# Kernel tuning notes

Hardware: AMD Instinct MI355X
Metric: run time of the kernel (lower is better)

## Reference

```python
import jax, jax.numpy as jnp
import numpy as np
from math import sqrt

N = 50000
E = 800000
D_EMB = 512
DK = 64
DV = 64
HEADS = 8


def setup_inputs() -> dict:
    key = jax.random.key(0)
    k1, k2, k3, k4 = jax.random.split(key, 4)
    x = jax.random.normal(k1, (N, D_EMB), dtype=jnp.float32)
    edge_index = jax.random.randint(k2, (2, E), 0, N, dtype=jnp.int64)
    out_qkv = (2 * DK + DV) * HEADS  # 1536
    W_qkv = jax.random.normal(k3, (out_qkv, D_EMB), dtype=jnp.float32) / sqrt(D_EMB)
    b_qkv = jnp.zeros((out_qkv,), dtype=jnp.float32)
    W_ff = jax.random.normal(k4, (D_EMB, DV * HEADS), dtype=jnp.float32) / sqrt(DV * HEADS)
    b_ff = jnp.zeros((D_EMB,), dtype=jnp.float32)
    return {"x": x, "edge_index": edge_index, "W_qkv": W_qkv, "b_qkv": b_qkv,
            "W_ff": W_ff, "b_ff": b_ff}


def _attention_message(Q, K, V, senders, receivers, n_nodes):
    # Q,K: [N, H, dK], V: [N, H, dV]; edge lists: [E]
    scale = 1.0 / sqrt(Q.shape[-1])
    # per-edge scores: [E, H]
    scores = jnp.einsum('ehd,ehd->eh', Q[receivers], K[senders]) * scale
    # segment softmax over incoming edges of each receiver
    smax = jax.ops.segment_max(scores, receivers, num_segments=n_nodes)  # [N, H]
    ex = jnp.exp(scores - smax[receivers])                               # [E, H]
    denom = jax.ops.segment_sum(ex, receivers, num_segments=n_nodes)    # [N, H]
    att = ex / denom[receivers]                                         # [E, H]
    # weighted scatter of V from senders to receivers: [N, H, dV]
    out = jax.ops.segment_sum(att[:, :, None] * V[senders], receivers,
                              num_segments=n_nodes)
    return out, att


def reference(x, edge_index, W_qkv, b_qkv, W_ff, b_ff):
    n_nodes = x.shape[0]
    qkv = x @ W_qkv.T + b_qkv  # [N, (2*dK+dV)*H]
    Q, K, V = jnp.split(qkv, [DK * HEADS, 2 * DK * HEADS], axis=-1)
    Q = Q.reshape(n_nodes, HEADS, DK)
    K = K.reshape(n_nodes, HEADS, DK)
    V = V.reshape(n_nodes, HEADS, DV)
    senders, receivers = edge_index[0], edge_index[1]
    msg, _ = _attention_message(Q, K, V, senders, receivers, n_nodes)
    # aggregate_heads: flatten heads and project to d_Embedding
    out = msg.reshape(n_nodes, HEADS * DV) @ W_ff.T + b_ff
    return out
```

## Files before the change

### kernel.cpp

```cpp
#include <hip/hip_runtime.h>

static constexpr int NN = 50000;
static constexpr int NE = 800000;
static constexpr int DEMB = 512;
static constexpr int QKV_OUT = 1536;

typedef _Float16 half8 __attribute__((ext_vector_type(8)));
typedef float floatx4 __attribute__((ext_vector_type(4)));

#define KQ_SCALE (127.0f / 5.5f)
#define KQ_DEQ   (5.5f / 127.0f)

static constexpr size_t OFF_QH   = 0;
static constexpr size_t OFF_KV8  = 51200000;
static constexpr size_t OFF_MSG  = 102400000;
static constexpr size_t OFF_SRT  = 153600000;
static constexpr size_t OFF_DEG  = 156800000;
static constexpr size_t OFF_OFFA = 157000000;
static constexpr size_t OFF_CUR  = 157200064;
static constexpr size_t OFF_FLAG = 157400064;
static constexpr size_t OFF_WQH  = 157400128;
static constexpr size_t OFF_WFH  = 158972992;

typedef __attribute__((address_space(1))) const void* gas_ptr;
typedef __attribute__((address_space(3))) void* lds_ptr_t;

__device__ __forceinline__ void load_lds16(const void* g, void* l) {
  __builtin_amdgcn_global_load_lds((gas_ptr)g, (lds_ptr_t)l, 16, 0, 0);
}

__global__ __launch_bounds__(256)
void k_cvt(const float* __restrict__ in, _Float16* __restrict__ out, int n8) {
  int i = blockIdx.x * 256 + threadIdx.x;
  if (i < n8) {
    floatx4 a = *(const floatx4*)(in + (size_t)i * 8);
    floatx4 b = *(const floatx4*)(in + (size_t)i * 8 + 4);
    half8 h;
    #pragma unroll
    for (int q = 0; q < 4; ++q) { h[q] = (_Float16)a[q]; h[q + 4] = (_Float16)b[q]; }
    *(half8*)(out + (size_t)i * 8) = h;
  }
}

__global__ __launch_bounds__(64)
void k_detect64(const void* __restrict__ edge, int* __restrict__ flag) {
  if (threadIdx.x == 0) {
    const int* p = (const int*)edge;
    int is64 = 1;
    for (int i = 0; i < 16; ++i) if (p[2 * i + 1] != 0) is64 = 0;
    *flag = is64;
  }
}

__device__ __forceinline__ int edge_at(const void* edge, int row, int e, int is64) {
  if (is64) return (int)((const long long*)edge)[(size_t)row * NE + e];
  return ((const int*)edge)[(size_t)row * NE + e];
}

__global__ __launch_bounds__(1024)
void k_scan(const int* __restrict__ deg, int* __restrict__ off,
            int* __restrict__ cur, int n) {
  __shared__ int sums[1024];
  int tid = threadIdx.x;
  int per = (n + 1023) >> 10;
  int start = tid * per;
  int end = start + per; if (end > n) end = n;
  int s = 0;
  for (int i = start; i < end; ++i) s += deg[i];
  sums[tid] = s;
  __syncthreads();
  for (int d = 1; d < 1024; d <<= 1) {
    int v = (tid >= d) ? sums[tid - d] : 0;
    __syncthreads();
    sums[tid] += v;
    __syncthreads();
  }
  int run = (tid == 0) ? 0 : sums[tid - 1];
  for (int i = start; i < end; ++i) {
    off[i] = run; cur[i] = run; run += deg[i];
  }
  if (tid == 0) off[n] = sums[1023];
}

__global__ __launch_bounds__(256)
void k_scatter(const void* __restrict__ edge, const int* __restrict__ flag,
               int* __restrict__ cur, int* __restrict__ srt) {
  int e = blockIdx.x * 256 + threadIdx.x;
  if (e < NE) {
    int is64 = *flag;
    int r = edge_at(edge, 1, e, is64);
    int s = edge_at(edge, 0, e, is64);
    int pos = atomicAdd(&cur[r], 1);
    srt[pos] = s;
  }
}

template<int MODE>
__global__ __launch_bounds__(512, 2)
void k_gemmB(const _Float16* __restrict__ Ah, const _Float16* __restrict__ Bh,
             const float* __restrict__ bias,
             void* __restrict__ out0, void* __restrict__ out1,
             const void* __restrict__ edge, const int* __restrict__ flag,
             int* __restrict__ deg,
             int M, int N, int K, int nxt, int gemmBlocks) {
  __shared__ _Float16 Bs[128 * 512];
  const int tid = threadIdx.x;

  if (MODE == 0 && blockIdx.x >= gemmBlocks) {
    int e = (blockIdx.x - gemmBlocks) * 512 + tid;
    if (e < NE) {
      int r = edge_at(edge, 1, e, *flag);
      atomicAdd(&deg[r], 1);
    }
    return;
  }

  const int cpx = gemmBlocks >> 3;
  const int w = (blockIdx.x & 7) * cpx + (blockIdx.x >> 3);
  const int m0 = (w / nxt) * 512;
  const int n0 = (w % nxt) * 128;

  const int wid = tid >> 6, lane = tid & 63;
  const int fr = lane & 15;
  const int fs = lane >> 4;

  #pragma unroll
  for (int it = 0; it < 16; ++it) {
    int L = it * 512 + tid;
    int row = L >> 6, sc = L & 63;
    int c = sc ^ (row & 7);
    load_lds16(Bh + (size_t)(n0 + row) * K + c * 8, (char*)Bs + (size_t)L * 16);
  }

  floatx4 acc[4][8];
  #pragma unroll
  for (int m = 0; m < 4; ++m)
    #pragma unroll
    for (int n = 0; n < 8; ++n)
      #pragma unroll
      for (int q = 0; q < 4; ++q) acc[m][n][q] = 0.f;

  int arow[4];
  #pragma unroll
  for (int m = 0; m < 4; ++m) {
    int r = m0 + wid * 64 + m * 16 + fr;
    arow[m] = r < M ? r : M - 1;
  }

  __syncthreads();

  auto LDA = [&](half8* dst, int t) {
    const int k0 = t * 32 + fs * 8;
    #pragma unroll
    for (int m = 0; m < 4; ++m)
      dst[m] = *(const half8*)(Ah + (size_t)arow[m] * K + k0);
  };

  half8 a[4], an[4];
  LDA(a, 0);
  for (int t = 0; t < 16; ++t) {
    if (t + 1 < 16) LDA(an, t + 1);
    half8 b[8];
    #pragma unroll
    for (int n = 0; n < 8; ++n) {
      int R = n * 16 + fr;
      int c = (t * 4 + fs) ^ (R & 7);
      b[n] = *(const half8*)(Bs + R * 512 + c * 8);
    }
    #pragma unroll
    for (int m = 0; m < 4; ++m)
      #pragma unroll
      for (int n = 0; n < 8; ++n)
        acc[m][n] = __builtin_amdgcn_mfma_f32_16x16x32_f16(a[m], b[n], acc[m][n], 0, 0, 0);
    #pragma unroll
    for (int m = 0; m < 4; ++m) a[m] = an[m];
  }

  const int fq = fs << 2;
  #pragma unroll
  for (int m = 0; m < 4; ++m) {
    #pragma unroll
    for (int n = 0; n < 8; ++n) {
      int gn = n0 + n * 16 + fr;
      float bv = bias[gn];
      #pragma unroll
      for (int q = 0; q < 4; ++q) {
        int gm = m0 + wid * 64 + m * 16 + fq + q;
        if (gm < M) {
          float val = acc[m][n][q] + bv;
          if (MODE == 0) {
            int region = gn >> 9;
            int d = gn & 511;
            if (region == 0) {
              ((_Float16*)out0)[(size_t)gm * 512 + d] = (_Float16)val;
            } else {
              float s = fminf(fmaxf(val * KQ_SCALE, -127.f), 127.f);
              signed char c = (signed char)__float2int_rn(s);
              size_t idx = (size_t)gm * 1024 + ((d >> 3) << 4) + (d & 7)
                         + (region == 2 ? 8 : 0);
              ((signed char*)out1)[idx] = c;
            }
          } else {
            ((float*)out0)[(size_t)gm * N + gn] = val;
          }
        }
      }
    }
  }
}

__global__ __launch_bounds__(256)
void k_attn(const _Float16* __restrict__ Qh, const unsigned char* __restrict__ KV8,
            const int* __restrict__ off, const int* __restrict__ srt,
            _Float16* __restrict__ msg) {
  int r = blockIdx.x * 4 + (threadIdx.x >> 6);
  if (r >= NN) return;
  int lane = threadIdx.x & 63;
  int qoff = lane * 8;

  half8 qh = *(const half8*)(Qh + (size_t)r * 512 + qoff);
  float q[8];
  #pragma unroll
  for (int i = 0; i < 8; ++i) q[i] = (float)qh[i] * 0.125f * KQ_DEQ;

  float denom = 0.f;
  float acc[8];
  #pragma unroll
  for (int i = 0; i < 8; ++i) acc[i] = 0.f;

  int e0 = off[r], e1 = off[r + 1];
  if (e1 <= e0) {
    half8 z = {};
    *(half8*)(msg + (size_t)r * 512 + qoff) = z;
    return;
  }

  auto gload = [&](uint4& kv, int s) {
    kv = *(const uint4*)(KV8 + (size_t)s * 1024 + lane * 16);
  };
  auto consume = [&](uint4 kv) {
    int xw = (int)kv.x, yw = (int)kv.y;
    float p = 0.f;
    p += q[0] * (float)((xw << 24) >> 24);
    p += q[1] * (float)((xw << 16) >> 24);
    p += q[2] * (float)((xw << 8) >> 24);
    p += q[3] * (float)(xw >> 24);
    p += q[4] * (float)((yw << 24) >> 24);
    p += q[5] * (float)((yw << 16) >> 24);
    p += q[6] * (float)((yw << 8) >> 24);
    p += q[7] * (float)(yw >> 24);
    p += __shfl_xor(p, 1);
    p += __shfl_xor(p, 2);
    p += __shfl_xor(p, 4);
    float w = __expf(p);
    denom += w;
    int vx = (int)kv.z, vy = (int)kv.w;
    acc[0] += w * (float)((vx << 24) >> 24);
    acc[1] += w * (float)((vx << 16) >> 24);
    acc[2] += w * (float)((vx << 8) >> 24);
    acc[3] += w * (float)(vx >> 24);
    acc[4] += w * (float)((vy << 24) >> 24);
    acc[5] += w * (float)((vy << 16) >> 24);
    acc[6] += w * (float)((vy << 8) >> 24);
    acc[7] += w * (float)(vy >> 24);
  };
  auto sidx = [&](int e) { return srt[e < e1 ? e : e1 - 1]; };

  uint4 b0, b1, b2, b3;
  gload(b0, sidx(e0));
  gload(b1, sidx(e0 + 1));
  gload(b2, sidx(e0 + 2));
  gload(b3, sidx(e0 + 3));
  int sn0 = sidx(e0 + 4), sn1 = sidx(e0 + 5), sn2 = sidx(e0 + 6), sn3 = sidx(e0 + 7);

  int e = e0;
  for (; e + 4 <= e1; e += 4) {
    consume(b0); gload(b0, sn0);
    consume(b1); gload(b1, sn1);
    consume(b2); gload(b2, sn2);
    consume(b3); gload(b3, sn3);
    sn0 = sidx(e + 8); sn1 = sidx(e + 9); sn2 = sidx(e + 10); sn3 = sidx(e + 11);
  }
  int rem = e1 - e;
  if (rem > 0) consume(b0);
  if (rem > 1) consume(b1);
  if (rem > 2) consume(b2);

  float inv = KQ_DEQ / denom;
  half8 oh;
  #pragma unroll
  for (int i = 0; i < 8; ++i) oh[i] = (_Float16)(acc[i] * inv);
  *(half8*)(msg + (size_t)r * 512 + qoff) = oh;
}

extern "C" void kernel_launch(void* const* d_in, const int* in_sizes, int n_in,
                              void* d_out, int out_size, void* d_ws, size_t ws_size,
                              hipStream_t stream) {
  const float* x     = (const float*)d_in[0];
  const void*  edge  = d_in[1];
  const float* W_qkv = (const float*)d_in[2];
  const float* b_qkv = (const float*)d_in[3];
  const float* W_ff  = (const float*)d_in[4];
  const float* b_ff  = (const float*)d_in[5];
  float* out = (float*)d_out;

  char* ws = (char*)d_ws;
  _Float16* Qh = (_Float16*)(ws + OFF_QH);
  unsigned char* KV8 = (unsigned char*)(ws + OFF_KV8);
  _Float16* msgb = (_Float16*)(ws + OFF_MSG);
  _Float16* xh   = (_Float16*)(ws + OFF_MSG);
  int* srt  = (int*)(ws + OFF_SRT);
  int* deg  = (int*)(ws + OFF_DEG);
  int* offa = (int*)(ws + OFF_OFFA);
  int* cur  = (int*)(ws + OFF_CUR);
  int* flag = (int*)(ws + OFF_FLAG);
  _Float16* wqh = (_Float16*)(ws + OFF_WQH);
  _Float16* wfh = (_Float16*)(ws + OFF_WFH);

  hipMemsetAsync(deg, 0, NN * sizeof(int), stream);
  k_detect64<<<1, 64, 0, stream>>>(edge, flag);

  k_cvt<<<(NN * DEMB / 8 + 255) / 256, 256, 0, stream>>>(x, xh, NN * DEMB / 8);
  k_cvt<<<(QKV_OUT * DEMB / 8 + 255) / 256, 256, 0, stream>>>(W_qkv, wqh, QKV_OUT * DEMB / 8);
  k_cvt<<<(DEMB * DEMB / 8 + 255) / 256, 256, 0, stream>>>(W_ff, wfh, DEMB * DEMB / 8);

  const int gemmBlocks = 1176;
  const int histoBlocks = (NE + 511) / 512;
  k_gemmB<0><<<gemmBlocks + histoBlocks, 512, 0, stream>>>(
      xh, wqh, b_qkv, Qh, KV8, edge, flag, deg,
      NN, QKV_OUT, DEMB, 12, gemmBlocks);

  k_scan<<<1, 1024, 0, stream>>>(deg, offa, cur, NN);
  k_scatter<<<(NE + 255) / 256, 256, 0, stream>>>(edge, flag, cur, srt);

  k_attn<<<(NN + 3) / 4, 256, 0, stream>>>(Qh, KV8, offa, srt, msgb);

  k_gemmB<1><<<392, 512, 0, stream>>>(
      msgb, wfh, b_ff, out, nullptr, nullptr, nullptr, nullptr,
      NN, DEMB, DEMB, 4, 392);
}
```

Measured before the change: 542.8 us.

## Make GEMM blocks persistent over M tiles with 64-wide B panels; merge conversions

```diff
diff --git a/kernel.cpp b/kernel.cpp
--- a/kernel.cpp
+++ b/kernel.cpp
@@ -30,16 +30,23 @@
 }
 
 __global__ __launch_bounds__(256)
-void k_cvt(const float* __restrict__ in, _Float16* __restrict__ out, int n8) {
+void k_cvt3(const float* __restrict__ x, const float* __restrict__ wq,
+            const float* __restrict__ wf,
+            _Float16* __restrict__ xh, _Float16* __restrict__ wqh,
+            _Float16* __restrict__ wfh) {
+  const int A8 = NN * DEMB / 8, B8 = QKV_OUT * DEMB / 8, C8 = DEMB * DEMB / 8;
   int i = blockIdx.x * 256 + threadIdx.x;
-  if (i < n8) {
-    floatx4 a = *(const floatx4*)(in + (size_t)i * 8);
-    floatx4 b = *(const floatx4*)(in + (size_t)i * 8 + 4);
-    half8 h;
-    #pragma unroll
-    for (int q = 0; q < 4; ++q) { h[q] = (_Float16)a[q]; h[q + 4] = (_Float16)b[q]; }
-    *(half8*)(out + (size_t)i * 8) = h;
-  }
+  const float* in; _Float16* out; int j;
+  if (i < A8)           { in = x;  out = xh;  j = i; }
+  else if (i < A8 + B8) { in = wq; out = wqh; j = i - A8; }
+  else if (i < A8 + B8 + C8) { in = wf; out = wfh; j = i - A8 - B8; }
+  else return;
+  floatx4 a = *(const floatx4*)(in + (size_t)j * 8);
+  floatx4 b = *(const floatx4*)(in + (size_t)j * 8 + 4);
+  half8 h;
+  #pragma unroll
+  for (int q = 0; q < 4; ++q) { h[q] = (_Float16)a[q]; h[q + 4] = (_Float16)b[q]; }
+  *(half8*)(out + (size_t)j * 8) = h;
 }
 
 __global__ __launch_bounds__(64)
@@ -96,14 +103,14 @@
 }
 
 template<int MODE>
-__global__ __launch_bounds__(512, 2)
-void k_gemmB(const _Float16* __restrict__ Ah, const _Float16* __restrict__ Bh,
+__global__ __launch_bounds__(512, 4)
+void k_gemmP(const _Float16* __restrict__ Ah, const _Float16* __restrict__ Bh,
              const float* __restrict__ bias,
              void* __restrict__ out0, void* __restrict__ out1,
              const void* __restrict__ edge, const int* __restrict__ flag,
              int* __restrict__ deg,
-             int M, int N, int K, int nxt, int gemmBlocks) {
-  __shared__ _Float16 Bs[128 * 512];
+             int M, int K, int NPANEL, int NG, int MT, int gemmBlocks) {
+  __shared__ _Float16 Bs[64 * 512];
   const int tid = threadIdx.x;
 
   if (MODE == 0 && blockIdx.x >= gemmBlocks) {
@@ -117,91 +124,93 @@
 
   const int cpx = gemmBlocks >> 3;
   const int w = (blockIdx.x & 7) * cpx + (blockIdx.x >> 3);
-  const int m0 = (w / nxt) * 512;
-  const int n0 = (w % nxt) * 128;
-
-  const int wid = tid >> 6, lane = tid & 63;
-  const int fr = lane & 15;
-  const int fs = lane >> 4;
-
-  #pragma unroll
-  for (int it = 0; it < 16; ++it) {
+  const int g = w / NPANEL;
+  const int n0 = (w % NPANEL) * 64;
+
+  #pragma unroll
+  for (int it = 0; it < 8; ++it) {
     int L = it * 512 + tid;
     int row = L >> 6, sc = L & 63;
     int c = sc ^ (row & 7);
     load_lds16(Bh + (size_t)(n0 + row) * K + c * 8, (char*)Bs + (size_t)L * 16);
   }
 
-  floatx4 acc[4][8];
-  #pragma unroll
-  for (int m = 0; m < 4; ++m)
+  const int wid = tid >> 6, lane = tid & 63;
+  const int fr = lane & 15;
+  const int fs = lane >> 4;
+
+  __syncthreads();
+
+  for (int mt = g; mt < MT; mt += NG) {
+    int arow[4];
     #pragma unroll
-    for (int n = 0; n < 8; ++n)
-      #pragma unroll
-      for (int q = 0; q < 4; ++q) acc[m][n][q] = 0.f;
-
-  int arow[4];
-  #pragma unroll
-  for (int m = 0; m < 4; ++m) {
-    int r = m0 + wid * 64 + m * 16 + fr;
-    arow[m] = r < M ? r : M - 1;
-  }
-
-  __syncthreads();
-
-  auto LDA = [&](half8* dst, int t) {
-    const int k0 = t * 32 + fs * 8;
+    for (int m = 0; m < 4; ++m) {
+      int r = mt * 512 + wid * 64 + m * 16 + fr;
+      arow[m] = r < M ? r : M - 1;
+    }
+
+    floatx4 acc[4][4];
     #pragma unroll
     for (int m = 0; m < 4; ++m)
-      dst[m] = *(const half8*)(Ah + (size_t)arow[m] * K + k0);
-  };
-
-  half8 a[4], an[4];
-  LDA(a, 0);
-  for (int t = 0; t < 16; ++t) {
-    if (t + 1 < 16) LDA(an, t + 1);
-    half8 b[8];
+      #pragma unroll
+      for (int n = 0; n < 4; ++n)
+        #pragma unroll
+        for (int q = 0; q < 4; ++q) acc[m][n][q] = 0.f;
+
+    auto LDA = [&](half8* dst, int t) {
+      const int k0 = t * 32 + fs * 8;
+      #pragma unroll
+      for (int m = 0; m < 4; ++m)
+        dst[m] = *(const half8*)(Ah + (size_t)arow[m] * K + k0);
+    };
+
+    half8 a[4], an[4];
+    LDA(a, 0);
+    for (int t = 0; t < 16; ++t) {
+      if (t + 1 < 16) LDA(an, t + 1);
+      half8 b[4];
+      #pragma unroll
+      for (int n = 0; n < 4; ++n) {
+        int R = n * 16 + fr;
+        int sc = (t * 4 + fs) ^ (R & 7);
+        b[n] = *(const half8*)(Bs + R * 512 + sc * 8);
+      }
+      #pragma unroll
+      for (int m = 0; m < 4; ++m)
+        #pragma unroll
+        for (int n = 0; n < 4; ++n)
+          acc[m][n] = __builtin_amdgcn_mfma_f32_16x16x32_f16(a[m], b[n], acc[m][n], 0, 0, 0);
+      #pragma unroll
+      for (int m = 0; m < 4; ++m) a[m] = an[m];
+    }
+
+    const int fq = fs << 2;
     #pragma unroll
-    for (int n = 0; n < 8; ++n) {
-      int R = n * 16 + fr;
-      int c = (t * 4 + fs) ^ (R & 7);
-      b[n] = *(const half8*)(Bs + R * 512 + c * 8);
-    }
-    #pragma unroll
-    for (int m = 0; m < 4; ++m)
-      #pragma unroll
-      for (int n = 0; n < 8; ++n)
-        acc[m][n] = __builtin_amdgcn_mfma_f32_16x16x32_f16(a[m], b[n], acc[m][n], 0, 0, 0);
-    #pragma unroll
-    for (int m = 0; m < 4; ++m) a[m] = an[m];
-  }
-
-  const int fq = fs << 2;
-  #pragma unroll
-  for (int m = 0; m < 4; ++m) {
-    #pragma unroll
-    for (int n = 0; n < 8; ++n) {
-      int gn = n0 + n * 16 + fr;
-      float bv = bias[gn];
-      #pragma unroll
-      for (int q = 0; q < 4; ++q) {
-        int gm = m0 + wid * 64 + m * 16 + fq + q;
-        if (gm < M) {
-          float val = acc[m][n][q] + bv;
-          if (MODE == 0) {
-            int region = gn >> 9;
-            int d = gn & 511;
-            if (region == 0) {
-              ((_Float16*)out0)[(size_t)gm * 512 + d] = (_Float16)val;
+    for (int m = 0; m < 4; ++m) {
+      #pragma unroll
+      for (int n = 0; n < 4; ++n) {
+        int gn = n0 + n * 16 + fr;
+        float bv = bias[gn];
+        #pragma unroll
+        for (int q = 0; q < 4; ++q) {
+          int gm = mt * 512 + wid * 64 + m * 16 + fq + q;
+          if (gm < M) {
+            float val = acc[m][n][q] + bv;
+            if (MODE == 0) {
+              int region = gn >> 9;
+              int d = gn & 511;
+              if (region == 0) {
+                ((_Float16*)out0)[(size_t)gm * 512 + d] = (_Float16)val;
+              } else {
+                float s = fminf(fmaxf(val * KQ_SCALE, -127.f), 127.f);
+                signed char c = (signed char)__float2int_rn(s);
+                size_t idx = (size_t)gm * 1024 + ((d >> 3) << 4) + (d & 7)
+                           + (region == 2 ? 8 : 0);
+                ((signed char*)out1)[idx] = c;
+              }
             } else {
-              float s = fminf(fmaxf(val * KQ_SCALE, -127.f), 127.f);
-              signed char c = (signed char)__float2int_rn(s);
-              size_t idx = (size_t)gm * 1024 + ((d >> 3) << 4) + (d & 7)
-                         + (region == 2 ? 8 : 0);
-              ((signed char*)out1)[idx] = c;
+              ((float*)out0)[(size_t)gm * 512 + gn] = val;
             }
-          } else {
-            ((float*)out0)[(size_t)gm * N + gn] = val;
           }
         }
       }
@@ -320,22 +329,21 @@
   hipMemsetAsync(deg, 0, NN * sizeof(int), stream);
   k_detect64<<<1, 64, 0, stream>>>(edge, flag);
 
-  k_cvt<<<(NN * DEMB / 8 + 255) / 256, 256, 0, stream>>>(x, xh, NN * DEMB / 8);
-  k_cvt<<<(QKV_OUT * DEMB / 8 + 255) / 256, 256, 0, stream>>>(W_qkv, wqh, QKV_OUT * DEMB / 8);
-  k_cvt<<<(DEMB * DEMB / 8 + 255) / 256, 256, 0, stream>>>(W_ff, wfh, DEMB * DEMB / 8);
-
-  const int gemmBlocks = 1176;
+  const int cvtN = NN * DEMB / 8 + QKV_OUT * DEMB / 8 + DEMB * DEMB / 8;
+  k_cvt3<<<(cvtN + 255) / 256, 256, 0, stream>>>(x, W_qkv, W_ff, xh, wqh, wfh);
+
+  const int gemmBlocks = 504;
   const int histoBlocks = (NE + 511) / 512;
-  k_gemmB<0><<<gemmBlocks + histoBlocks, 512, 0, stream>>>(
+  k_gemmP<0><<<gemmBlocks + histoBlocks, 512, 0, stream>>>(
       xh, wqh, b_qkv, Qh, KV8, edge, flag, deg,
-      NN, QKV_OUT, DEMB, 12, gemmBlocks);
+      NN, DEMB, 24, 21, 98, gemmBlocks);
 
   k_scan<<<1, 1024, 0, stream>>>(deg, offa, cur, NN);
   k_scatter<<<(NE + 255) / 256, 256, 0, stream>>>(edge, flag, cur, srt);
 
   k_attn<<<(NN + 3) / 4, 256, 0, stream>>>(Qh, KV8, offa, srt, msgb);
 
-  k_gemmB<1><<<392, 512, 0, stream>>>(
+  k_gemmP<1><<<256, 512, 0, stream>>>(
       msgb, wfh, b_ff, out, nullptr, nullptr, nullptr, nullptr,
-      NN, DEMB, DEMB, 4, 392);
-}
+      NN, DEMB, 8, 32, 98, 256);
+}
```

Measured after the change: 693.4 us. 27.7% more time.
